# Kernel tuning notes

Measured on AMD Instinct MI355X. Metric: run time of the kernel, lower is better.

The kernel has to match this reference:

```python
import math
import jax, jax.numpy as jnp
import numpy as np

B, T, E, H = 2, 2048, 1024, 16
HS = E // H  # head size = 64
NEG = jnp.float32(-1e10)


def setup_inputs() -> dict:
    key = jax.random.key(0)
    ks = jax.random.split(key, 7)
    return {
        "query": jax.random.normal(ks[0], (B, T, E), jnp.float32),
        "key": jax.random.normal(ks[1], (B, T, E), jnp.float32),
        "value": jax.random.normal(ks[2], (B, T, E), jnp.float32),
        "Wq": jax.random.normal(ks[3], (E, E), jnp.float32) * 0.02,
        "Wk": jax.random.normal(ks[4], (E, E), jnp.float32) * 0.02,
        "Wv": jax.random.normal(ks[5], (E, E), jnp.float32) * 0.02,
        "Wp": jax.random.normal(ks[6], (E, E), jnp.float32) * 0.02,
    }


def reference(query, key, value, Wq, Wk, Wv, Wp):
    # QKV projections (no bias), split into heads: [B, H, T, HS]
    q = (query @ Wq).reshape(B, T, H, HS).transpose(0, 2, 1, 3)
    k = (key @ Wk).reshape(B, T, H, HS).transpose(0, 2, 1, 3)
    v = (value @ Wv).reshape(B, T, H, HS).transpose(0, 2, 1, 3)
    # scaled dot-product scores [B, H, T, T]
    att = jnp.einsum("bhqd,bhkd->bhqk", q, k) / math.sqrt(HS)
    # additive causal mask (tril allowed)
    causal = jnp.tril(jnp.ones((T, T), dtype=att.dtype))
    att = att + jnp.where(causal == 0, NEG, jnp.float32(0.0))[None, None]
    att = jax.nn.softmax(att, axis=-1)
    # dropout rate 0 / deterministic -> identity
    y = jnp.einsum("bhqk,bhkd->bhqd", att, v)
    y = y.transpose(0, 2, 1, 3).reshape(B, T, E)
    y = y @ Wp
    return y
```

## Files before the change

kernel.cpp:

```cpp
#include <hip/hip_runtime.h>

#define TB 2
#define TT 2048
#define TE 1024
#define TH 16
#define THS 64
#define TM (TB * TT)

typedef __attribute__((ext_vector_type(8))) short short8;
typedef __attribute__((ext_vector_type(4))) float f32x4;
typedef __attribute__((ext_vector_type(16))) float f32x16;

__device__ __forceinline__ f32x4 mfma16(short8 a, short8 b, f32x4 c) {
    return __builtin_amdgcn_mfma_f32_16x16x32_bf16(a, b, c, 0, 0, 0);
}
__device__ __forceinline__ f32x16 mfma32(short8 a, short8 b, f32x16 c) {
    return __builtin_amdgcn_mfma_f32_32x32x16_bf16(a, b, c, 0, 0, 0);
}

__device__ __forceinline__ void gload_lds16(const void* g, void* l) {
    __builtin_amdgcn_global_load_lds(
        (const __attribute__((address_space(1))) void*)g,
        (__attribute__((address_space(3))) void*)l, 16, 0, 0);
}

__device__ __forceinline__ unsigned short f2bf(float f) {
    unsigned int u = __float_as_uint(f);
    u += 0x7fff + ((u >> 16) & 1);
    return (unsigned short)(u >> 16);
}

__device__ __forceinline__ unsigned cvtpk_bf16(float lo, float hi) {
    unsigned r;
    asm("v_cvt_pk_bf16_f32 %0, %1, %2" : "=v"(r) : "v"(lo), "v"(hi));
    return r;
}
__device__ __forceinline__ void plswap(unsigned& a, unsigned& b) {
    asm("v_permlane32_swap_b32 %0, %1" : "+v"(a), "+v"(b));
}

__global__ __launch_bounds__(256) void prep(
    const float* __restrict__ q, const float* __restrict__ k,
    const float* __restrict__ v, unsigned short* __restrict__ qc,
    unsigned short* __restrict__ kc, unsigned short* __restrict__ vc,
    const float* __restrict__ W0, const float* __restrict__ W1,
    const float* __restrict__ W2, const float* __restrict__ W3,
    unsigned short* __restrict__ T0, unsigned short* __restrict__ T1,
    unsigned short* __restrict__ T2, unsigned short* __restrict__ T3) {
    __shared__ float Ts[32][33];
    const int y = blockIdx.y;
    if (y < 3) {
        const float* src = (y == 0) ? q : (y == 1) ? k : v;
        unsigned short* dst = (y == 0) ? qc : (y == 1) ? kc : vc;
        const int i = blockIdx.x * 256 + threadIdx.x;
        float4 vv = ((const float4*)src)[i];
        ushort4 o;
        o.x = f2bf(vv.x); o.y = f2bf(vv.y); o.z = f2bf(vv.z); o.w = f2bf(vv.w);
        ((ushort4*)dst)[i] = o;
    } else {
        const int x = blockIdx.x;
        const int z = x >> 10, rem = x & 1023;
        const float* W = (z == 0) ? W0 : (z == 1) ? W1 : (z == 2) ? W2 : W3;
        unsigned short* Wt = (z == 0) ? T0 : (z == 1) ? T1 : (z == 2) ? T2 : T3;
        const int r0 = ((rem >> 5) & 31) * 32, c0 = (rem & 31) * 32;
        const int t = threadIdx.x;
        const int r = t >> 3, c = (t & 7) * 4;
        float4 vv = *(const float4*)&W[(size_t)(r0 + r) * TE + c0 + c];
        Ts[r][c] = vv.x; Ts[r][c + 1] = vv.y; Ts[r][c + 2] = vv.z; Ts[r][c + 3] = vv.w;
        __syncthreads();
        ushort4 o;
        o.x = f2bf(Ts[c + 0][r]); o.y = f2bf(Ts[c + 1][r]);
        o.z = f2bf(Ts[c + 2][r]); o.w = f2bf(Ts[c + 3][r]);
        *(ushort4*)&Wt[(size_t)(c0 + r) * TE + r0 + c] = o;
    }
}

__global__ __launch_bounds__(256, 2) void gemm_qkv(
    const unsigned short* __restrict__ qc, const unsigned short* __restrict__ kc,
    const unsigned short* __restrict__ vc, const unsigned short* __restrict__ Wqt,
    const unsigned short* __restrict__ Wkt, const unsigned short* __restrict__ Wvt,
    unsigned short* __restrict__ Qb, unsigned short* __restrict__ Kb,
    unsigned short* __restrict__ Vt) {
    __shared__ unsigned short LDS[32768];

    const int lin = blockIdx.x;
    const int swz = (lin & 7) * 96 + (lin >> 3);
    const int z = swz >> 8;
    const int rem = swz & 255;
    const int bm = (rem & 31) * 128, bn = (rem >> 5) * 128;

    const unsigned short* A  = (z == 0) ? qc : (z == 1) ? kc : vc;
    const unsigned short* Bt = (z == 0) ? Wqt : (z == 1) ? Wkt : Wvt;

    const int tid = threadIdx.x;
    const int w = tid >> 6, lane = tid & 63;
    const int quad = lane >> 4, l16 = lane & 15;
    const int wm = (w >> 1) * 64, wn = (w & 1) * 64;

    const int srow = lane >> 2;
    const int scol = (((lane & 3) ^ ((srow >> 1) & 3))) * 8;
    const int rchunk = (quad ^ ((l16 >> 1) & 3)) * 8;

    f32x4 acc[4][4];
    const f32x4 fz = {0.f, 0.f, 0.f, 0.f};
    #pragma unroll
    for (int i = 0; i < 4; ++i)
        #pragma unroll
        for (int j = 0; j < 4; ++j) acc[i][j] = fz;

    auto stageA = [&](int t, int half) {
        const int buf = t & 1, k0 = t * 64;
        #pragma unroll
        for (int j = 0; j < 2; ++j) {
            const int e = w * 2 + j;
            const int kk = e >> 2, i2 = e & 3;
            const int cr = half * 2 + (i2 & 1) + ((i2 >> 1) << 2);
            gload_lds16(A + (size_t)(bm + cr * 16 + srow) * TE + k0 + kk * 32 + scol,
                        &LDS[buf * 8192 + kk * 4096 + cr * 512 + lane * 8]);
        }
    };
    auto stageB = [&](int t, int half) {
        const int buf = t & 1, k0 = t * 64;
        #pragma unroll
        for (int j = 0; j < 2; ++j) {
            const int e = w * 2 + j;
            const int kk = e >> 2, i2 = e & 3;
            const int cc = half * 2 + (i2 & 1) + ((i2 >> 1) << 2);
            gload_lds16(Bt + (size_t)(bn + cc * 16 + srow) * TE + k0 + kk * 32 + scol,
                        &LDS[16384 + buf * 8192 + kk * 4096 + cc * 512 + lane * 8]);
        }
    };

    auto ktile = [&](int t, bool st, bool last) {
        const int buf = t & 1;
        const unsigned short* Al = &LDS[buf * 8192];
        const unsigned short* Bl = &LDS[16384 + buf * 8192];
        short8 af[2][2], blo[2][2], bhi[2][2];
        #pragma unroll
        for (int mi = 0; mi < 2; ++mi)
            #pragma unroll
            for (int kk = 0; kk < 2; ++kk)
                af[mi][kk] = *(const short8*)&Al[kk * 4096 + ((w >> 1) * 4 + mi) * 512 + l16 * 32 + rchunk];
        #pragma unroll
        for (int nj = 0; nj < 2; ++nj)
            #pragma unroll
            for (int kk = 0; kk < 2; ++kk)
                blo[nj][kk] = *(const short8*)&Bl[kk * 4096 + ((w & 1) * 4 + nj) * 512 + l16 * 32 + rchunk];
        asm volatile("s_waitcnt lgkmcnt(0)" ::: "memory");
        __builtin_amdgcn_sched_barrier(0);
        __builtin_amdgcn_s_setprio(1);
        #pragma unroll
        for (int mi = 0; mi < 2; ++mi)
            #pragma unroll
            for (int nj = 0; nj < 2; ++nj)
                #pragma unroll
                for (int kk = 0; kk < 2; ++kk)
                    acc[mi][nj] = mfma16(af[mi][kk], blo[nj][kk], acc[mi][nj]);
        __builtin_amdgcn_s_setprio(0);
        __builtin_amdgcn_sched_barrier(0);
        __builtin_amdgcn_s_barrier();
        #pragma unroll
        for (int nj = 0; nj < 2; ++nj)
            #pragma unroll
            for (int kk = 0; kk < 2; ++kk)
                bhi[nj][kk] = *(const short8*)&Bl[kk * 4096 + ((w & 1) * 4 + 2 + nj) * 512 + l16 * 32 + rchunk];
        if (st) { stageA(t + 2, 0); stageB(t + 2, 0); }
        asm volatile("s_waitcnt lgkmcnt(0)" ::: "memory");
        __builtin_amdgcn_sched_barrier(0);
        __builtin_amdgcn_s_setprio(1);
        #pragma unroll
        for (int mi = 0; mi < 2; ++mi)
            #pragma unroll
            for (int nj = 0; nj < 2; ++nj)
                #pragma unroll
                for (int kk = 0; kk < 2; ++kk)
                    acc[mi][2 + nj] = mfma16(af[mi][kk], bhi[nj][kk], acc[mi][2 + nj]);
        __builtin_amdgcn_s_setprio(0);
        __builtin_amdgcn_sched_barrier(0);
        __builtin_amdgcn_s_barrier();
        #pragma unroll
        for (int mi = 0; mi < 2; ++mi)
            #pragma unroll
            for (int kk = 0; kk < 2; ++kk)
                af[mi][kk] = *(const short8*)&Al[kk * 4096 + ((w >> 1) * 4 + 2 + mi) * 512 + l16 * 32 + rchunk];
        if (st) stageB(t + 2, 1);
        asm volatile("s_waitcnt lgkmcnt(0)" ::: "memory");
        __builtin_amdgcn_sched_barrier(0);
        __builtin_amdgcn_s_setprio(1);
        #pragma unroll
        for (int mi = 0; mi < 2; ++mi)
            #pragma unroll
            for (int nj = 0; nj < 2; ++nj)
                #pragma unroll
                for (int kk = 0; kk < 2; ++kk)
                    acc[2 + mi][nj] = mfma16(af[mi][kk], blo[nj][kk], acc[2 + mi][nj]);
        __builtin_amdgcn_s_setprio(0);
        __builtin_amdgcn_sched_barrier(0);
        __builtin_amdgcn_s_barrier();
        if (st) stageA(t + 2, 1);
        __builtin_amdgcn_s_setprio(1);
        #pragma unroll
        for (int mi = 0; mi < 2; ++mi)
            #pragma unroll
            for (int nj = 0; nj < 2; ++nj)
                #pragma unroll
                for (int kk = 0; kk < 2; ++kk)
                    acc[2 + mi][2 + nj] = mfma16(af[mi][kk], bhi[nj][kk], acc[2 + mi][2 + nj]);
        __builtin_amdgcn_s_setprio(0);
        __builtin_amdgcn_sched_barrier(0);
        if (st) {
            asm volatile("s_waitcnt vmcnt(8)" ::: "memory");
        } else if (last) {
            asm volatile("s_waitcnt vmcnt(0)" ::: "memory");
        }
        __builtin_amdgcn_s_barrier();
    };

    stageA(0, 0); stageB(0, 0); stageB(0, 1); stageA(0, 1);
    stageA(1, 0); stageB(1, 0); stageB(1, 1); stageA(1, 1);
    asm volatile("s_waitcnt vmcnt(8)" ::: "memory");
    __builtin_amdgcn_s_barrier();

    #pragma unroll 1
    for (int t = 0; t < 14; ++t) ktile(t, true, false);
    ktile(14, false, true);
    ktile(15, false, false);

    if (z < 2) {
        unsigned short* Cb = (z == 0) ? Qb : Kb;
        const float sc = (z == 0) ? 0.18033688011112042f : 1.0f;
        #pragma unroll
        for (int mi = 0; mi < 4; ++mi)
            #pragma unroll
            for (int nj = 0; nj < 4; ++nj) {
                const int m0 = bm + wm + mi * 16 + quad * 4;
                const int n = bn + wn + nj * 16 + l16;
                #pragma unroll
                for (int r = 0; r < 4; ++r)
                    Cb[(size_t)(m0 + r) * TE + n] = f2bf(acc[mi][nj][r] * sc);
            }
    } else {
        #pragma unroll
        for (int mi = 0; mi < 4; ++mi)
            #pragma unroll
            for (int nj = 0; nj < 4; ++nj) {
                const int m0 = bm + wm + mi * 16 + quad * 4;
                const int n = bn + wn + nj * 16 + l16;
                ushort4 o;
                o.x = f2bf(acc[mi][nj][0]); o.y = f2bf(acc[mi][nj][1]);
                o.z = f2bf(acc[mi][nj][2]); o.w = f2bf(acc[mi][nj][3]);
                size_t idx = ((size_t)((m0 >> 11) * TH + (n >> 6)) * THS + (n & 63)) * TT + (m0 & (TT - 1));
                *(ushort4*)&Vt[idx] = o;
            }
    }
}

__global__ __launch_bounds__(256, 2) void gemm_out(
    const unsigned short* __restrict__ A, const unsigned short* __restrict__ Bt,
    float* __restrict__ C) {
    __shared__ unsigned short As[2][128 * 32];
    __shared__ unsigned short Bs[2][64 * 32];

    const int tid = threadIdx.x;
    const int w = tid >> 6, lane = tid & 63;
    const int quad = lane >> 4, l16 = lane & 15;
    const int bm = blockIdx.x * 128, bn = blockIdx.y * 64;
    const int wm = (w >> 1) * 64, wn = (w & 1) * 32;

    f32x4 acc[4][2];
    const f32x4 fz = {0.f, 0.f, 0.f, 0.f};
    #pragma unroll
    for (int i = 0; i < 4; ++i)
        #pragma unroll
        for (int j = 0; j < 2; ++j) acc[i][j] = fz;

    const int srow = lane >> 2;
    const int scol = (((lane & 3) ^ ((srow >> 1) & 3))) * 8;
    const int rchunk = (quad ^ ((l16 >> 1) & 3)) * 8;

    auto stage = [&](int k0, int buf) {
        #pragma unroll
        for (int i = 0; i < 3; ++i) {
            const int ch = w * 3 + i;
            if (ch < 8)
                gload_lds16(A + (size_t)(bm + ch * 16 + srow) * TE + k0 + scol,
                            &As[buf][ch * 512 + lane * 8]);
            else
                gload_lds16(Bt + (size_t)(bn + (ch - 8) * 16 + srow) * TE + k0 + scol,
                            &Bs[buf][(ch - 8) * 512 + lane * 8]);
        }
    };

    stage(0, 0);
    int cur = 0;
    for (int k0 = 0; k0 < TE; k0 += 32) {
        __syncthreads();
        if (k0 + 32 < TE) stage(k0 + 32, cur ^ 1);

        short8 af[4], bf[2];
        #pragma unroll
        for (int i = 0; i < 4; ++i)
            af[i] = *(const short8*)&As[cur][(wm + i * 16 + l16) * 32 + rchunk];
        #pragma unroll
        for (int j = 0; j < 2; ++j)
            bf[j] = *(const short8*)&Bs[cur][(wn + j * 16 + l16) * 32 + rchunk];
        #pragma unroll
        for (int i = 0; i < 4; ++i)
            #pragma unroll
            for (int j = 0; j < 2; ++j)
                acc[i][j] = mfma16(af[i], bf[j], acc[i][j]);
        cur ^= 1;
    }

    #pragma unroll
    for (int i = 0; i < 4; ++i)
        #pragma unroll
        for (int j = 0; j < 2; ++j) {
            const int m0 = bm + wm + i * 16 + quad * 4;
            const int n = bn + wn + j * 16 + l16;
            #pragma unroll
            for (int r = 0; r < 4; ++r)
                C[(size_t)(m0 + r) * TE + n] = acc[i][j][r];
        }
}

__global__ __launch_bounds__(512, 2) void attn_mfma(
    const unsigned short* __restrict__ Q, const unsigned short* __restrict__ K,
    const unsigned short* __restrict__ Vt, unsigned short* __restrict__ O) {
    __shared__ unsigned short S[49152];
    __shared__ float L0[128];

    const int tid = threadIdx.x;
    const int lane = tid & 63;
    const int wv = tid >> 6;
    const int wk = wv >> 2;
    const int wl = wv & 3;
    const int rl = lane & 31, x = lane >> 5;

    const int lin = blockIdx.x;
    const int bh = lin & 31;
    const int p = lin >> 5;
    const int b = bh >> 4, h = bh & 15;
    const int itA = 15 - p, itB = p;
    const int hA = itA + 1, hB = itB + 1;

    const unsigned short* Kg = K + (size_t)b * TT * TE + h * THS;
    const unsigned short* Vg = Vt + (size_t)bh * THS * TT;

    short8 aqA[4], aqB[4];
    {
        const size_t rA = (size_t)(b * TT + itA * 128 + wl * 32 + rl) * TE + h * THS + x * 8;
        const size_t rB = (size_t)(b * TT + itB * 128 + wl * 32 + rl) * TE + h * THS + x * 8;
        #pragma unroll
        for (int c = 0; c < 4; ++c) {
            aqA[c] = *(const short8*)&Q[rA + c * 16];
            aqB[c] = *(const short8*)&Q[rB + c * 16];
        }
    }

    const int srow = lane >> 2;
    const int scol = (((lane & 3) ^ ((srow >> 1) & 3))) * 8;
    unsigned short* Sg = S + wk * 24576;

    auto stage = [&](int jt, int buf) {
        const int k0 = jt * 64;
        if (wl < 2) {
            #pragma unroll
            for (int j = 0; j < 4; ++j) {
                const int ee = wl * 4 + j;
                const int kk = ee >> 2, r16 = (ee & 3) * 16;
                gload_lds16(Kg + (size_t)(k0 + r16 + srow) * TE + kk * 32 + scol,
                            &Sg[buf * 4096 + ee * 512 + lane * 8]);
            }
        } else {
            #pragma unroll
            for (int j = 0; j < 4; ++j) {
                const int ee = (wl - 2) * 4 + j;
                const int kk = ee >> 2, r16 = (ee & 3) * 16;
                gload_lds16(Vg + (size_t)(r16 + srow) * TT + k0 + kk * 32 + scol,
                            &Sg[12288 + buf * 4096 + ee * 512 + lane * 8]);
            }
        }
    };
    auto stageS = [&](int s) {
        if (s >= 17) return;
        const int it = (s < hA) ? itA : itB;
        const int loc = (s < hA) ? s : s - hA;
        const int jt = (wk ? it + 1 : 0) + loc;
        stage(jt, s % 3);
    };

    stageS(0); stageS(1);

    const int xr = (rl >> 1) & 3;

    auto run_seg = [&](int it, const short8* aq, int sBase, int hSeg) {
        const int q0 = it * 128;
        const int qv = q0 + wl * 32 + rl;
        const int qwMin = q0 + wl * 32;
        f32x16 accO0, accO1;
        #pragma unroll
        for (int i = 0; i < 16; ++i) { accO0[i] = 0.f; accO1[i] = 0.f; }
        float lacc = 0.f;

        for (int i = 0; i < hSeg; ++i) {
            const int s = sBase + i;
            const int buf = s % 3;
            if (s == 16) { asm volatile("s_waitcnt vmcnt(0)" ::: "memory"); }
            else         { asm volatile("s_waitcnt vmcnt(4)" ::: "memory"); }
            __builtin_amdgcn_s_barrier();
            __builtin_amdgcn_sched_barrier(0);
            stageS(s + 2);

            const int jt = (wk ? it + 1 : 0) + i;
            const int k0 = jt * 64;
            const unsigned short* Kb = &Sg[buf * 4096];
            const unsigned short* Vb = &Sg[12288 + buf * 4096];

            f32x16 sa0, sa1;
            #pragma unroll
            for (int i2 = 0; i2 < 16; ++i2) { sa0[i2] = 0.f; sa1[i2] = 0.f; }
            #pragma unroll
            for (int c = 0; c < 4; ++c) {
                const int off = (c >> 1) * 2048 + ((((c & 1) * 2 + x) ^ xr)) * 8;
                short8 kf0 = *(const short8*)&Kb[off + rl * 32];
                short8 kf1 = *(const short8*)&Kb[off + (32 + rl) * 32];
                sa0 = mfma32(kf0, aq[c], sa0);
                sa1 = mfma32(kf1, aq[c], sa1);
            }

            const bool open = (k0 + 63 <= qwMin);
            short8 pb[4];
            #pragma unroll
            for (int mt = 0; mt < 2; ++mt) {
                float pv[16];
                #pragma unroll
                for (int r = 0; r < 16; ++r) {
                    const float sv = (mt == 0) ? sa0[r] : sa1[r];
                    float e = __builtin_amdgcn_exp2f(sv);
                    if (!open) {
                        const int kg = k0 + mt * 32 + (r & 3) + 8 * (r >> 2) + 4 * x;
                        e = (kg > qv) ? 0.f : e;
                    }
                    pv[r] = e;
                    lacc += e;
                }
                unsigned w0 = cvtpk_bf16(pv[0], pv[1]),   w1 = cvtpk_bf16(pv[2], pv[3]);
                unsigned w2 = cvtpk_bf16(pv[4], pv[5]),   w3 = cvtpk_bf16(pv[6], pv[7]);
                unsigned w4 = cvtpk_bf16(pv[8], pv[9]),   w5 = cvtpk_bf16(pv[10], pv[11]);
                unsigned w6 = cvtpk_bf16(pv[12], pv[13]), w7 = cvtpk_bf16(pv[14], pv[15]);
                plswap(w0, w2); plswap(w1, w3);
                plswap(w4, w6); plswap(w5, w7);
                union { unsigned u[4]; short8 s8; } f0, f1;
                f0.u[0] = w0; f0.u[1] = w1; f0.u[2] = w2; f0.u[3] = w3;
                f1.u[0] = w4; f1.u[1] = w5; f1.u[2] = w6; f1.u[3] = w7;
                pb[mt * 2] = f0.s8; pb[mt * 2 + 1] = f1.s8;
            }

            __builtin_amdgcn_s_setprio(1);
            #pragma unroll
            for (int c = 0; c < 4; ++c) {
                const int off = (c >> 1) * 2048 + ((((c & 1) * 2 + x) ^ xr)) * 8;
                short8 vf0 = *(const short8*)&Vb[off + rl * 32];
                short8 vf1 = *(const short8*)&Vb[off + (32 + rl) * 32];
                accO0 = mfma32(vf0, pb[c], accO0);
                accO1 = mfma32(vf1, pb[c], accO1);
            }
            __builtin_amdgcn_s_setprio(0);
        }

        lacc += __shfl_xor(lacc, 32);

        __syncthreads();
        const int lastS = sBase + hSeg - 1;
        const int fb = lastS % 3;
        if (wk == 0) {
            #pragma unroll
            for (int dt = 0; dt < 2; ++dt)
                #pragma unroll
                for (int q4 = 0; q4 < 4; ++q4) {
                    const int i16 = ((dt ^ ((lane >> 2) & 1)) << 4) + ((q4 ^ (lane & 3)) << 2);
                    const int flat = (wl * 64 + lane) * 32 + i16;
                    const int chunk = flat >> 11, offf = flat & 2047;
                    float* dst = (float*)&S[(chunk >> 1) * 24576 + (chunk & 1) * 12288 + fb * 4096] + offf;
                    float4 vstv;
                    if (dt == 0) { vstv.x = accO0[q4*4+0]; vstv.y = accO0[q4*4+1]; vstv.z = accO0[q4*4+2]; vstv.w = accO0[q4*4+3]; }
                    else         { vstv.x = accO1[q4*4+0]; vstv.y = accO1[q4*4+1]; vstv.z = accO1[q4*4+2]; vstv.w = accO1[q4*4+3]; }
                    *(float4*)dst = vstv;
                }
            if (lane < 32) L0[wl * 32 + rl] = lacc;
        }
        __syncthreads();
        if (wk == 1) {
            const float lf = lacc + L0[wl * 32 + rl];
            const float linv = 1.0f / lf;
            unsigned short* Og = O + (size_t)(b * TT + q0 + wl * 32 + rl) * TE + h * THS;
            #pragma unroll
            for (int dt = 0; dt < 2; ++dt)
                #pragma unroll
                for (int q4 = 0; q4 < 4; ++q4) {
                    const int i16 = ((dt ^ ((lane >> 2) & 1)) << 4) + ((q4 ^ (lane & 3)) << 2);
                    const int flat = (wl * 64 + lane) * 32 + i16;
                    const int chunk = flat >> 11, offf = flat & 2047;
                    const float4 vld = *(const float4*)((const float*)&S[(chunk >> 1) * 24576 + (chunk & 1) * 12288 + fb * 4096] + offf);
                    float o0, o1, o2, o3;
                    if (dt == 0) { o0 = accO0[q4*4+0] + vld.x; o1 = accO0[q4*4+1] + vld.y; o2 = accO0[q4*4+2] + vld.z; o3 = accO0[q4*4+3] + vld.w; }
                    else         { o0 = accO1[q4*4+0] + vld.x; o1 = accO1[q4*4+1] + vld.y; o2 = accO1[q4*4+2] + vld.z; o3 = accO1[q4*4+3] + vld.w; }
                    const int dbase = 8 * q4 + 4 * x + 32 * dt;
                    ushort4 o;
                    o.x = f2bf(o0 * linv); o.y = f2bf(o1 * linv);
                    o.z = f2bf(o2 * linv); o.w = f2bf(o3 * linv);
                    *(ushort4*)&Og[dbase] = o;
                }
        }
    };

    run_seg(itA, aqA, 0, hA);
    run_seg(itB, aqB, hA, hB);
}

extern "C" void kernel_launch(void* const* d_in, const int* in_sizes, int n_in,
                              void* d_out, int out_size, void* d_ws, size_t ws_size,
                              hipStream_t stream) {
    const float* q  = (const float*)d_in[0];
    const float* k  = (const float*)d_in[1];
    const float* v  = (const float*)d_in[2];
    const float* Wq = (const float*)d_in[3];
    const float* Wk = (const float*)d_in[4];
    const float* Wv = (const float*)d_in[5];
    const float* Wp = (const float*)d_in[6];
    float* out = (float*)d_out;

    const size_t se = (size_t)TM * TE;
    unsigned short* qc  = (unsigned short*)d_ws;
    unsigned short* kc  = qc + se;
    unsigned short* vc  = kc + se;
    unsigned short* Qb  = vc + se;
    unsigned short* Kb  = Qb + se;
    unsigned short* Vt  = Kb + se;
    unsigned short* Ob  = Vt + se;
    unsigned short* Wqt = Ob + se;
    unsigned short* Wkt = Wqt + (size_t)TE * TE;
    unsigned short* Wvt = Wkt + (size_t)TE * TE;
    unsigned short* Wpt = Wvt + (size_t)TE * TE;

    prep<<<dim3(4096, 4), 256, 0, stream>>>(q, k, v, qc, kc, vc,
                                            Wq, Wk, Wv, Wp, Wqt, Wkt, Wvt, Wpt);

    gemm_qkv<<<768, 256, 0, stream>>>(qc, kc, vc, Wqt, Wkt, Wvt, Qb, Kb, Vt);

    attn_mfma<<<256, 512, 0, stream>>>(Qb, Kb, Vt, Ob);

    gemm_out<<<dim3(TM / 128, TE / 64), 256, 0, stream>>>(Ob, Wpt, out);
}
```

Measured before the change: 206.7 us.

## Split paired q-tiles into separate blocks with double-buffered LDS and higher occupancy

The attention kernel no longer pairs a long and a short causal q-tile in one block. It launches one block per q-tile, doubling the grid to 512 blocks. LDS staging shrinks from triple to double buffering so that up to 4 blocks fit per CU, and the row-sum accumulation is split into four partial sums to shorten the add dependency chain. The goal is more parallelism and occupancy. The cost is uneven per-block work, which is left to the hardware scheduler, and a full vmcnt(0) wait every iteration, which reduces load/compute overlap.

```diff
diff --git a/kernel.cpp b/kernel.cpp
--- a/kernel.cpp
+++ b/kernel.cpp
@@ -324,10 +324,10 @@
         }
 }
 
-__global__ __launch_bounds__(512, 2) void attn_mfma(
+__global__ __launch_bounds__(512, 4) void attn_mfma(
     const unsigned short* __restrict__ Q, const unsigned short* __restrict__ K,
     const unsigned short* __restrict__ Vt, unsigned short* __restrict__ O) {
-    __shared__ unsigned short S[49152];
+    __shared__ unsigned short S[32768];
     __shared__ float L0[128];
 
     const int tid = threadIdx.x;
@@ -339,28 +339,24 @@
 
     const int lin = blockIdx.x;
     const int bh = lin & 31;
-    const int p = lin >> 5;
+    const int it = 15 - (lin >> 5);
     const int b = bh >> 4, h = bh & 15;
-    const int itA = 15 - p, itB = p;
-    const int hA = itA + 1, hB = itB + 1;
+    const int h0 = it + 1;
+    const int base = wk ? h0 : 0;
 
     const unsigned short* Kg = K + (size_t)b * TT * TE + h * THS;
     const unsigned short* Vg = Vt + (size_t)bh * THS * TT;
 
-    short8 aqA[4], aqB[4];
+    short8 aq[4];
     {
-        const size_t rA = (size_t)(b * TT + itA * 128 + wl * 32 + rl) * TE + h * THS + x * 8;
-        const size_t rB = (size_t)(b * TT + itB * 128 + wl * 32 + rl) * TE + h * THS + x * 8;
-        #pragma unroll
-        for (int c = 0; c < 4; ++c) {
-            aqA[c] = *(const short8*)&Q[rA + c * 16];
-            aqB[c] = *(const short8*)&Q[rB + c * 16];
-        }
+        const size_t rQ = (size_t)(b * TT + it * 128 + wl * 32 + rl) * TE + h * THS + x * 8;
+        #pragma unroll
+        for (int c = 0; c < 4; ++c) aq[c] = *(const short8*)&Q[rQ + c * 16];
     }
 
     const int srow = lane >> 2;
     const int scol = (((lane & 3) ^ ((srow >> 1) & 3))) * 8;
-    unsigned short* Sg = S + wk * 24576;
+    unsigned short* Sg = S + wk * 16384;
 
     auto stage = [&](int jt, int buf) {
         const int k0 = jt * 64;
@@ -378,145 +374,133 @@
                 const int ee = (wl - 2) * 4 + j;
                 const int kk = ee >> 2, r16 = (ee & 3) * 16;
                 gload_lds16(Vg + (size_t)(r16 + srow) * TT + k0 + kk * 32 + scol,
-                            &Sg[12288 + buf * 4096 + ee * 512 + lane * 8]);
+                            &Sg[8192 + buf * 4096 + ee * 512 + lane * 8]);
             }
         }
     };
-    auto stageS = [&](int s) {
-        if (s >= 17) return;
-        const int it = (s < hA) ? itA : itB;
-        const int loc = (s < hA) ? s : s - hA;
-        const int jt = (wk ? it + 1 : 0) + loc;
-        stage(jt, s % 3);
-    };
-
-    stageS(0); stageS(1);
+
+    stage(base, 0);
 
     const int xr = (rl >> 1) & 3;
-
-    auto run_seg = [&](int it, const short8* aq, int sBase, int hSeg) {
-        const int q0 = it * 128;
-        const int qv = q0 + wl * 32 + rl;
-        const int qwMin = q0 + wl * 32;
-        f32x16 accO0, accO1;
-        #pragma unroll
-        for (int i = 0; i < 16; ++i) { accO0[i] = 0.f; accO1[i] = 0.f; }
-        float lacc = 0.f;
-
-        for (int i = 0; i < hSeg; ++i) {
-            const int s = sBase + i;
-            const int buf = s % 3;
-            if (s == 16) { asm volatile("s_waitcnt vmcnt(0)" ::: "memory"); }
-            else         { asm volatile("s_waitcnt vmcnt(4)" ::: "memory"); }
-            __builtin_amdgcn_s_barrier();
-            __builtin_amdgcn_sched_barrier(0);
-            stageS(s + 2);
-
-            const int jt = (wk ? it + 1 : 0) + i;
-            const int k0 = jt * 64;
-            const unsigned short* Kb = &Sg[buf * 4096];
-            const unsigned short* Vb = &Sg[12288 + buf * 4096];
-
-            f32x16 sa0, sa1;
-            #pragma unroll
-            for (int i2 = 0; i2 < 16; ++i2) { sa0[i2] = 0.f; sa1[i2] = 0.f; }
-            #pragma unroll
-            for (int c = 0; c < 4; ++c) {
-                const int off = (c >> 1) * 2048 + ((((c & 1) * 2 + x) ^ xr)) * 8;
-                short8 kf0 = *(const short8*)&Kb[off + rl * 32];
-                short8 kf1 = *(const short8*)&Kb[off + (32 + rl) * 32];
-                sa0 = mfma32(kf0, aq[c], sa0);
-                sa1 = mfma32(kf1, aq[c], sa1);
-            }
-
-            const bool open = (k0 + 63 <= qwMin);
-            short8 pb[4];
-            #pragma unroll
-            for (int mt = 0; mt < 2; ++mt) {
-                float pv[16];
-                #pragma unroll
-                for (int r = 0; r < 16; ++r) {
-                    const float sv = (mt == 0) ? sa0[r] : sa1[r];
-                    float e = __builtin_amdgcn_exp2f(sv);
-                    if (!open) {
-                        const int kg = k0 + mt * 32 + (r & 3) + 8 * (r >> 2) + 4 * x;
-                        e = (kg > qv) ? 0.f : e;
-                    }
-                    pv[r] = e;
-                    lacc += e;
+    const int q0 = it * 128;
+    const int qv = q0 + wl * 32 + rl;
+    const int qwMin = q0 + wl * 32;
+
+    f32x16 accO0, accO1;
+    #pragma unroll
+    for (int i = 0; i < 16; ++i) { accO0[i] = 0.f; accO1[i] = 0.f; }
+    float lacc = 0.f;
+
+    #pragma unroll 1
+    for (int i = 0; i < h0; ++i) {
+        const int buf = i & 1;
+        asm volatile("s_waitcnt vmcnt(0)" ::: "memory");
+        __builtin_amdgcn_s_barrier();
+        __builtin_amdgcn_sched_barrier(0);
+        if (i + 1 < h0) stage(base + i + 1, buf ^ 1);
+
+        const int jt = base + i;
+        const int k0 = jt * 64;
+        const unsigned short* Kb = &Sg[buf * 4096];
+        const unsigned short* Vb = &Sg[8192 + buf * 4096];
+
+        f32x16 sa0, sa1;
+        #pragma unroll
+        for (int i2 = 0; i2 < 16; ++i2) { sa0[i2] = 0.f; sa1[i2] = 0.f; }
+        #pragma unroll
+        for (int c = 0; c < 4; ++c) {
+            const int off = (c >> 1) * 2048 + ((((c & 1) * 2 + x) ^ xr)) * 8;
+            short8 kf0 = *(const short8*)&Kb[off + rl * 32];
+            short8 kf1 = *(const short8*)&Kb[off + (32 + rl) * 32];
+            sa0 = mfma32(kf0, aq[c], sa0);
+            sa1 = mfma32(kf1, aq[c], sa1);
+        }
+
+        const bool open = (k0 + 63 <= qwMin);
+        short8 pb[4];
+        float lp0 = 0.f, lp1 = 0.f, lp2 = 0.f, lp3 = 0.f;
+        #pragma unroll
+        for (int mt = 0; mt < 2; ++mt) {
+            float pv[16];
+            #pragma unroll
+            for (int r = 0; r < 16; ++r) {
+                const float sv = (mt == 0) ? sa0[r] : sa1[r];
+                float e = __builtin_amdgcn_exp2f(sv);
+                if (!open) {
+                    const int kg = k0 + mt * 32 + (r & 3) + 8 * (r >> 2) + 4 * x;
+                    e = (kg > qv) ? 0.f : e;
                 }
-                unsigned w0 = cvtpk_bf16(pv[0], pv[1]),   w1 = cvtpk_bf16(pv[2], pv[3]);
-                unsigned w2 = cvtpk_bf16(pv[4], pv[5]),   w3 = cvtpk_bf16(pv[6], pv[7]);
-                unsigned w4 = cvtpk_bf16(pv[8], pv[9]),   w5 = cvtpk_bf16(pv[10], pv[11]);
-                unsigned w6 = cvtpk_bf16(pv[12], pv[13]), w7 = cvtpk_bf16(pv[14], pv[15]);
-                plswap(w0, w2); plswap(w1, w3);
-                plswap(w4, w6); plswap(w5, w7);
-                union { unsigned u[4]; short8 s8; } f0, f1;
-                f0.u[0] = w0; f0.u[1] = w1; f0.u[2] = w2; f0.u[3] = w3;
-                f1.u[0] = w4; f1.u[1] = w5; f1.u[2] = w6; f1.u[3] = w7;
-                pb[mt * 2] = f0.s8; pb[mt * 2 + 1] = f1.s8;
-            }
-
-            __builtin_amdgcn_s_setprio(1);
-            #pragma unroll
-            for (int c = 0; c < 4; ++c) {
-                const int off = (c >> 1) * 2048 + ((((c & 1) * 2 + x) ^ xr)) * 8;
-                short8 vf0 = *(const short8*)&Vb[off + rl * 32];
-                short8 vf1 = *(const short8*)&Vb[off + (32 + rl) * 32];
-                accO0 = mfma32(vf0, pb[c], accO0);
-                accO1 = mfma32(vf1, pb[c], accO1);
-            }
-            __builtin_amdgcn_s_setprio(0);
-        }
-
-        lacc += __shfl_xor(lacc, 32);
-
-        __syncthreads();
-        const int lastS = sBase + hSeg - 1;
-        const int fb = lastS % 3;
-        if (wk == 0) {
-            #pragma unroll
-            for (int dt = 0; dt < 2; ++dt)
-                #pragma unroll
-                for (int q4 = 0; q4 < 4; ++q4) {
-                    const int i16 = ((dt ^ ((lane >> 2) & 1)) << 4) + ((q4 ^ (lane & 3)) << 2);
-                    const int flat = (wl * 64 + lane) * 32 + i16;
-                    const int chunk = flat >> 11, offf = flat & 2047;
-                    float* dst = (float*)&S[(chunk >> 1) * 24576 + (chunk & 1) * 12288 + fb * 4096] + offf;
-                    float4 vstv;
-                    if (dt == 0) { vstv.x = accO0[q4*4+0]; vstv.y = accO0[q4*4+1]; vstv.z = accO0[q4*4+2]; vstv.w = accO0[q4*4+3]; }
-                    else         { vstv.x = accO1[q4*4+0]; vstv.y = accO1[q4*4+1]; vstv.z = accO1[q4*4+2]; vstv.w = accO1[q4*4+3]; }
-                    *(float4*)dst = vstv;
-                }
-            if (lane < 32) L0[wl * 32 + rl] = lacc;
-        }
-        __syncthreads();
-        if (wk == 1) {
-            const float lf = lacc + L0[wl * 32 + rl];
-            const float linv = 1.0f / lf;
-            unsigned short* Og = O + (size_t)(b * TT + q0 + wl * 32 + rl) * TE + h * THS;
-            #pragma unroll
-            for (int dt = 0; dt < 2; ++dt)
-                #pragma unroll
-                for (int q4 = 0; q4 < 4; ++q4) {
-                    const int i16 = ((dt ^ ((lane >> 2) & 1)) << 4) + ((q4 ^ (lane & 3)) << 2);
-                    const int flat = (wl * 64 + lane) * 32 + i16;
-                    const int chunk = flat >> 11, offf = flat & 2047;
-                    const float4 vld = *(const float4*)((const float*)&S[(chunk >> 1) * 24576 + (chunk & 1) * 12288 + fb * 4096] + offf);
-                    float o0, o1, o2, o3;
-                    if (dt == 0) { o0 = accO0[q4*4+0] + vld.x; o1 = accO0[q4*4+1] + vld.y; o2 = accO0[q4*4+2] + vld.z; o3 = accO0[q4*4+3] + vld.w; }
-                    else         { o0 = accO1[q4*4+0] + vld.x; o1 = accO1[q4*4+1] + vld.y; o2 = accO1[q4*4+2] + vld.z; o3 = accO1[q4*4+3] + vld.w; }
-                    const int dbase = 8 * q4 + 4 * x + 32 * dt;
-                    ushort4 o;
-                    o.x = f2bf(o0 * linv); o.y = f2bf(o1 * linv);
-                    o.z = f2bf(o2 * linv); o.w = f2bf(o3 * linv);
-                    *(ushort4*)&Og[dbase] = o;
-                }
-        }
-    };
-
-    run_seg(itA, aqA, 0, hA);
-    run_seg(itB, aqB, hA, hB);
+                pv[r] = e;
+                if ((r & 3) == 0) lp0 += e;
+                else if ((r & 3) == 1) lp1 += e;
+                else if ((r & 3) == 2) lp2 += e;
+                else lp3 += e;
+            }
+            unsigned w0 = cvtpk_bf16(pv[0], pv[1]),   w1 = cvtpk_bf16(pv[2], pv[3]);
+            unsigned w2 = cvtpk_bf16(pv[4], pv[5]),   w3 = cvtpk_bf16(pv[6], pv[7]);
+            unsigned w4 = cvtpk_bf16(pv[8], pv[9]),   w5 = cvtpk_bf16(pv[10], pv[11]);
+            unsigned w6 = cvtpk_bf16(pv[12], pv[13]), w7 = cvtpk_bf16(pv[14], pv[15]);
+            plswap(w0, w2); plswap(w1, w3);
+            plswap(w4, w6); plswap(w5, w7);
+            union { unsigned u[4]; short8 s8; } f0, f1;
+            f0.u[0] = w0; f0.u[1] = w1; f0.u[2] = w2; f0.u[3] = w3;
+            f1.u[0] = w4; f1.u[1] = w5; f1.u[2] = w6; f1.u[3] = w7;
+            pb[mt * 2] = f0.s8; pb[mt * 2 + 1] = f1.s8;
+        }
+        lacc += (lp0 + lp1) + (lp2 + lp3);
+
+        __builtin_amdgcn_s_setprio(1);
+        #pragma unroll
+        for (int c = 0; c < 4; ++c) {
+            const int off = (c >> 1) * 2048 + ((((c & 1) * 2 + x) ^ xr)) * 8;
+            short8 vf0 = *(const short8*)&Vb[off + rl * 32];
+            short8 vf1 = *(const short8*)&Vb[off + (32 + rl) * 32];
+            accO0 = mfma32(vf0, pb[c], accO0);
+            accO1 = mfma32(vf1, pb[c], accO1);
+        }
+        __builtin_amdgcn_s_setprio(0);
+    }
+
+    lacc += __shfl_xor(lacc, 32);
+
+    __syncthreads();
+    float* Sf = (float*)S;
+    if (wk == 0) {
+        #pragma unroll
+        for (int dt = 0; dt < 2; ++dt)
+            #pragma unroll
+            for (int q4 = 0; q4 < 4; ++q4) {
+                const int i16 = ((dt ^ ((lane >> 2) & 1)) << 4) + ((q4 ^ (lane & 3)) << 2);
+                const int flat = (wl * 64 + lane) * 32 + i16;
+                float4 vstv;
+                if (dt == 0) { vstv.x = accO0[q4*4+0]; vstv.y = accO0[q4*4+1]; vstv.z = accO0[q4*4+2]; vstv.w = accO0[q4*4+3]; }
+                else         { vstv.x = accO1[q4*4+0]; vstv.y = accO1[q4*4+1]; vstv.z = accO1[q4*4+2]; vstv.w = accO1[q4*4+3]; }
+                *(float4*)&Sf[flat] = vstv;
+            }
+        if (lane < 32) L0[wl * 32 + rl] = lacc;
+    }
+    __syncthreads();
+    if (wk == 1) {
+        const float lf = lacc + L0[wl * 32 + rl];
+        const float linv = 1.0f / lf;
+        unsigned short* Og = O + (size_t)(b * TT + q0 + wl * 32 + rl) * TE + h * THS;
+        #pragma unroll
+        for (int dt = 0; dt < 2; ++dt)
+            #pragma unroll
+            for (int q4 = 0; q4 < 4; ++q4) {
+                const int i16 = ((dt ^ ((lane >> 2) & 1)) << 4) + ((q4 ^ (lane & 3)) << 2);
+                const int flat = (wl * 64 + lane) * 32 + i16;
+                const float4 vld = *(const float4*)&Sf[flat];
+                float o0, o1, o2, o3;
+                if (dt == 0) { o0 = accO0[q4*4+0] + vld.x; o1 = accO0[q4*4+1] + vld.y; o2 = accO0[q4*4+2] + vld.z; o3 = accO0[q4*4+3] + vld.w; }
+                else         { o0 = accO1[q4*4+0] + vld.x; o1 = accO1[q4*4+1] + vld.y; o2 = accO1[q4*4+2] + vld.z; o3 = accO1[q4*4+3] + vld.w; }
+                const int dbase = 8 * q4 + 4 * x + 32 * dt;
+                ushort4 o;
+                o.x = f2bf(o0 * linv); o.y = f2bf(o1 * linv);
+                o.z = f2bf(o2 * linv); o.w = f2bf(o3 * linv);
+                *(ushort4*)&Og[dbase] = o;
+            }
+    }
 }
 
 extern "C" void kernel_launch(void* const* d_in, const int* in_sizes, int n_in,
@@ -549,7 +533,7 @@
 
     gemm_qkv<<<768, 256, 0, stream>>>(qc, kc, vc, Wqt, Wkt, Wvt, Qb, Kb, Vt);
 
-    attn_mfma<<<256, 512, 0, stream>>>(Qb, Kb, Vt, Ob);
+    attn_mfma<<<512, 512, 0, stream>>>(Qb, Kb, Vt, Ob);
 
     gemm_out<<<dim3(TM / 128, TE / 64), 256, 0, stream>>>(Ob, Wpt, out);
 }
```

New measurement: 208.0 us. Within noise of the previous version (+0.6%).
